# Kernel optimization log

Hardware: AMD Instinct MI355X
Metric: run time of the kernel (lower is better)

Reference implementation:

```python
import jax, jax.numpy as jnp
import numpy as np

B, N, D, H = 4, 1024, 1024, 16
DK = D // H
NEG_INF = jnp.finfo(jnp.float32).min


def setup_inputs() -> dict:
    key = jax.random.key(0)
    ks = jax.random.split(key, 6)
    x = jax.random.normal(ks[0], (B, N, D), dtype=jnp.float32)
    # padding mask: True where padded; vary lengths per batch element
    lengths = jnp.array([N, N - 128, N - 256, N - 512], dtype=jnp.int32)
    mask = jnp.arange(N)[None, :] >= lengths[:, None]  # [B, N] bool
    s = (1.0 / np.sqrt(D)).astype(np.float32)  # xavier-ish scale
    Wq = jax.random.normal(ks[1], (D, D), dtype=jnp.float32) * s
    Wk = jax.random.normal(ks[2], (D, D), dtype=jnp.float32) * s
    Wv = jax.random.normal(ks[3], (D, D), dtype=jnp.float32) * s
    Wo = jax.random.normal(ks[4], (D, D), dtype=jnp.float32) * s
    z = jnp.zeros((D,), dtype=jnp.float32)
    return {"x": x, "mask": mask, "Wq": Wq, "bq": z, "Wk": Wk, "bk": z,
            "Wv": Wv, "bv": z, "Wo": Wo, "bo": z}


def reference(x, mask, Wq, bq, Wk, bk, Wv, bv, Wo, bo):
    b, n, d = x.shape
    scale = jnp.asarray(DK, x.dtype) ** -0.5
    # QKV projections (weights stored [out, in] like torch Linear)
    def proj(W, bias):
        y = jnp.einsum('bnd,ed->bne', x, W) + bias
        return y.reshape(b, n, H, DK).transpose(0, 2, 1, 3)  # [B,H,N,Dk]
    q = proj(Wq, bq)
    k = proj(Wk, bk)
    v = proj(Wv, bv)
    energy = jnp.einsum('bhqd,bhkd->bhqk', q, k) * scale  # [B,H,N,N]
    energy = jnp.where(mask[:, None, None, :], NEG_INF, energy)
    weights = jax.nn.softmax(energy, axis=-1)
    attn = jnp.einsum('bhqk,bhkd->bhqd', weights, v)  # [B,H,N,Dk]
    attn = attn.transpose(0, 2, 1, 3).reshape(b, n, d)
    return jnp.einsum('bnd,ed->bne', attn, Wo) + bo
```

## Files before the change

kernel.cpp:

```cpp
#include <hip/hip_runtime.h>

#define DEV __device__ __forceinline__

typedef __attribute__((ext_vector_type(8))) short s16x8;
typedef __attribute__((ext_vector_type(4))) float f32x4;
typedef __attribute__((ext_vector_type(4))) unsigned short u16x4;
typedef __attribute__((ext_vector_type(2))) unsigned int u32x2;

static constexpr int Bb = 4, Nn = 1024, Dd = 1024, Hh = 16, DKk = 64;

DEV unsigned short f2bf(float f) {
    union { float f; unsigned int u; } x; x.f = f;
    unsigned int r = x.u + 0x7FFFu + ((x.u >> 16) & 1u);
    return (unsigned short)(r >> 16);
}

DEV float fexp2(float x) {
#if __has_builtin(__builtin_amdgcn_exp2f)
    return __builtin_amdgcn_exp2f(x);
#else
    return exp2f(x);
#endif
}

DEV void gld16(const void* g, void* l) {
    __builtin_amdgcn_global_load_lds(
        (const __attribute__((address_space(1))) void*)g,
        (__attribute__((address_space(3))) void*)l, 16, 0, 0);
}

DEV void wait_vm4_barrier() {
    __builtin_amdgcn_sched_barrier(0);
    asm volatile("s_waitcnt vmcnt(4)" ::: "memory");
    __builtin_amdgcn_sched_barrier(0);
    __builtin_amdgcn_s_barrier();
}

__global__ __launch_bounds__(256) void cast_k(const float* __restrict__ x,
                                              const float* __restrict__ Wq,
                                              const float* __restrict__ Wk,
                                              const float* __restrict__ Wv,
                                              const float* __restrict__ Wo,
                                              const unsigned int* __restrict__ mraw,
                                              unsigned short* __restrict__ xb,
                                              unsigned short* __restrict__ Wqb,
                                              unsigned short* __restrict__ Wkb,
                                              unsigned short* __restrict__ Wvb,
                                              unsigned short* __restrict__ Wob,
                                              int* __restrict__ lengths) {
    if (blockIdx.x == 4096) {
        __shared__ int is_u8;
        const int tid = threadIdx.x;
        if (tid == 0) is_u8 = 0;
        __syncthreads();
        int nz = 0;
        for (int i = tid; i < 1024; i += 256) nz |= (mraw[i] != 0u) ? 1 : 0;
        if (nz) is_u8 = 1;
        __syncthreads();
        const int wv = tid >> 6, lane = tid & 63;
        int cnt = 0;
        if (is_u8) {
            const unsigned char* b8 = (const unsigned char*)mraw;
            for (int n = lane; n < Nn; n += 64) cnt += (b8[wv * Nn + n] == 0) ? 1 : 0;
        } else {
            for (int n = lane; n < Nn; n += 64) cnt += (mraw[wv * Nn + n] == 0u) ? 1 : 0;
        }
#pragma unroll
        for (int off = 32; off; off >>= 1) cnt += __shfl_xor(cnt, off);
        if (lane == 0) lengths[wv] = cnt;
        return;
    }
    const size_t i = ((size_t)blockIdx.x * 256 + threadIdx.x) * 8;
    const float* src;
    unsigned short* dst;
    size_t off;
    const size_t XE = (size_t)4 * 1024 * 1024, WE = (size_t)1024 * 1024;
    if (i < XE) {
        src = x; dst = xb; off = i;
    } else {
        size_t j = i - XE;
        int w = (int)(j >> 20);
        off = j & (WE - 1);
        src = (w == 0) ? Wq : (w == 1) ? Wk : (w == 2) ? Wv : Wo;
        dst = (w == 0) ? Wqb : (w == 1) ? Wkb : (w == 2) ? Wvb : Wob;
    }
    f32x4 a = *(const f32x4*)(src + off);
    f32x4 b = *(const f32x4*)(src + off + 4);
    s16x8 t;
    t[0] = (short)f2bf(a[0]); t[1] = (short)f2bf(a[1]);
    t[2] = (short)f2bf(a[2]); t[3] = (short)f2bf(a[3]);
    t[4] = (short)f2bf(b[0]); t[5] = (short)f2bf(b[1]);
    t[6] = (short)f2bf(b[2]); t[7] = (short)f2bf(b[3]);
    *(s16x8*)(dst + off) = t;
}

DEV void gemm_kloop(const unsigned short* __restrict__ A,
                    const unsigned short* __restrict__ W,
                    char* lA, char* lB, int bm, int bn,
                    int tid, int kstep0, f32x4 (&acc)[4][4]) {
    const int wv = tid >> 6, lane = tid & 63, g = lane >> 4, lr = lane & 15;
    const int wr = wv >> 1, wc = wv & 1;

    const int rbase = wv * 8 + (lane >> 3);
    const int corig = (lane & 7) ^ (lane >> 3);
    const unsigned short* Asrc = A + (size_t)(bm + rbase) * Dd + corig * 8;
    const unsigned short* Bsrc = W + (size_t)(bn + rbase) * Dd + corig * 8;
    const int ldsb = wv * 1024;
    const int xk = (lr & 7);

    int kstep = kstep0;
    for (int it = 0; it < 16; ++it) {
        const int k0 = kstep * 64;
#pragma unroll
        for (int p = 0; p < 4; ++p) {
            gld16(Asrc + (size_t)(p * 32) * Dd + k0, lA + p * 4096 + ldsb);
            gld16(Bsrc + (size_t)(p * 32) * Dd + k0, lB + p * 4096 + ldsb);
        }
        __syncthreads();
#pragma unroll
        for (int s = 0; s < 2; ++s) {
            s16x8 af[4], bf[4];
#pragma unroll
            for (int m = 0; m < 4; ++m)
                af[m] = *(const s16x8*)(lA + (wr * 64 + m * 16 + lr) * 128 + (((s * 4 + g) ^ xk) << 4));
#pragma unroll
            for (int n = 0; n < 4; ++n)
                bf[n] = *(const s16x8*)(lB + (wc * 64 + n * 16 + lr) * 128 + (((s * 4 + g) ^ xk) << 4));
#pragma unroll
            for (int m = 0; m < 4; ++m)
#pragma unroll
                for (int n = 0; n < 4; ++n)
                    acc[m][n] = __builtin_amdgcn_mfma_f32_16x16x32_bf16(af[m], bf[n], acc[m][n], 0, 0, 0);
        }
        __syncthreads();
        kstep = (kstep + 1) & 15;
    }
}

__global__ __launch_bounds__(256, 4) void gemm_qkv_k(const unsigned short* __restrict__ xb,
                                                     const unsigned short* __restrict__ Wqb,
                                                     const unsigned short* __restrict__ Wkb,
                                                     const unsigned short* __restrict__ Wvb,
                                                     const float* __restrict__ bq,
                                                     const float* __restrict__ bk,
                                                     const float* __restrict__ bv,
                                                     unsigned short* __restrict__ Qo,
                                                     unsigned short* __restrict__ Ko,
                                                     unsigned short* __restrict__ Vo) {
    __shared__ __align__(16) char lA[128 * 64 * 2];
    __shared__ __align__(16) char lB[128 * 64 * 2];
    const int z = blockIdx.z;
    const unsigned short* W = (z == 0) ? Wqb : (z == 1) ? Wkb : Wvb;
    const float* bias = (z == 0) ? bq : (z == 1) ? bk : bv;

    const int tid = threadIdx.x;
    const int wv = tid >> 6, lane = tid & 63, g = lane >> 4, lr = lane & 15;
    const int wr = wv >> 1, wc = wv & 1;
    const int bm = blockIdx.x * 128, bn = blockIdx.y * 128;
    const int kstep0 = (blockIdx.x * 5 + blockIdx.y * 3 + z * 7) & 15;

    f32x4 acc[4][4];
#pragma unroll
    for (int m = 0; m < 4; ++m)
#pragma unroll
        for (int n = 0; n < 4; ++n) acc[m][n] = (f32x4){0.f, 0.f, 0.f, 0.f};

    gemm_kloop(xb, W, lA, lB, bm, bn, tid, kstep0, acc);

    const int row0 = bm + wr * 64 + g * 4;
    if (z == 0) {
        const float qs = 0.125f * 1.44269504f;
#pragma unroll
        for (int m = 0; m < 4; ++m)
#pragma unroll
            for (int n = 0; n < 4; ++n) {
                const int col = bn + wc * 64 + n * 16 + lr;
                const float bv_ = bias[col];
#pragma unroll
                for (int r = 0; r < 4; ++r)
                    Qo[(size_t)(row0 + m * 16 + r) * Dd + col] = f2bf((acc[m][n][r] + bv_) * qs);
            }
    } else if (z == 1) {
#pragma unroll
        for (int m = 0; m < 4; ++m)
#pragma unroll
            for (int n = 0; n < 4; ++n) {
                const int col = bn + wc * 64 + n * 16 + lr;
                const int h = col >> 6, dk = col & 63;
                const float bv_ = bias[col];
#pragma unroll
                for (int r = 0; r < 4; ++r) {
                    const int rowg = row0 + m * 16 + r;
                    const int b_ = rowg >> 10, tok = rowg & 1023;
                    size_t idx = ((size_t)(b_ * Hh + h) * Nn + tok) * DKk +
                                 (((dk >> 3) ^ (tok & 7)) << 3) + (dk & 7);
                    Ko[idx] = f2bf(acc[m][n][r] + bv_);
                }
            }
    } else {
#pragma unroll
        for (int m = 0; m < 4; ++m)
#pragma unroll
            for (int n = 0; n < 4; ++n) {
                const int col = bn + wc * 64 + n * 16 + lr;
                const int h = col >> 6, dk = col & 63;
                const float bv_ = bias[col];
                const int rowg = row0 + m * 16;
                const int b_ = rowg >> 10, tok = rowg & 1023;
                u16x4 t;
#pragma unroll
                for (int r = 0; r < 4; ++r) t[r] = f2bf(acc[m][n][r] + bv_);
                size_t idx = ((size_t)(b_ * Hh + h) * DKk + dk) * Nn + (tok & ~63) +
                             ((((tok >> 3) & 7) ^ (dk & 7)) << 3) + (tok & 7);
                *(u16x4*)(Vo + idx) = t;
            }
    }
}

__global__ __launch_bounds__(256, 4) void gemm_out_k(const unsigned short* __restrict__ Ab,
                                                     const unsigned short* __restrict__ Wob,
                                                     const float* __restrict__ bo,
                                                     float* __restrict__ out) {
    __shared__ __align__(16) char lA[128 * 64 * 2];
    __shared__ __align__(16) char lB[128 * 64 * 2];
    const int tid = threadIdx.x;
    const int wv = tid >> 6, lane = tid & 63, g = lane >> 4, lr = lane & 15;
    const int wr = wv >> 1, wc = wv & 1;
    const int bm = blockIdx.x * 128, bn = blockIdx.y * 128;
    const int kstep0 = (blockIdx.x * 5 + blockIdx.y * 3) & 15;

    f32x4 acc[4][4];
#pragma unroll
    for (int m = 0; m < 4; ++m)
#pragma unroll
        for (int n = 0; n < 4; ++n) acc[m][n] = (f32x4){0.f, 0.f, 0.f, 0.f};

    gemm_kloop(Ab, Wob, lA, lB, bm, bn, tid, kstep0, acc);

    const int row0 = bm + wr * 64 + g * 4;
#pragma unroll
    for (int m = 0; m < 4; ++m)
#pragma unroll
        for (int n = 0; n < 4; ++n) {
            const int col = bn + wc * 64 + n * 16 + lr;
            const float bv_ = bo[col];
#pragma unroll
            for (int r = 0; r < 4; ++r)
                out[(size_t)(row0 + m * 16 + r) * Dd + col] = acc[m][n][r] + bv_;
        }
}

__global__ __launch_bounds__(256) void attn_k(const unsigned short* __restrict__ Q,
                                              const unsigned short* __restrict__ Kg,
                                              const unsigned short* __restrict__ Vtg,
                                              const int* __restrict__ lengths,
                                              unsigned short* __restrict__ O) {
    const int tid = threadIdx.x;
    const int wv = tid >> 6, lane = tid & 63, g = lane >> 4, lr = lane & 15;
    const int bid = blockIdx.x;
    const int qt = bid & 15, h = (bid >> 4) & 15, b = bid >> 8;
    const int len = lengths[b];
    const int nt = (len + 63) >> 6;

    __shared__ __align__(16) char Ks[2 * 64 * 128];
    __shared__ __align__(16) char Vs[2 * 64 * 128];
    __shared__ __align__(16) char Ps[4][16 * 128];

    s16x8 qf[2];
    {
        const int qrow = b * Nn + qt * 64 + wv * 16 + lr;
        const unsigned short* qp = Q + (size_t)qrow * Dd + h * DKk + g * 8;
        qf[0] = *(const s16x8*)qp;
        qf[1] = *(const s16x8*)(qp + 32);
    }

    float m_run = 0.f, l_run = 0.f;
    f32x4 oacc[4];
#pragma unroll
    for (int dt = 0; dt < 4; ++dt) oacc[dt] = (f32x4){0.f, 0.f, 0.f, 0.f};

    const int s0 = wv * 64 + lane;
    const int r0 = s0 >> 3, c0 = s0 & 7;
    const int r1 = r0 + 32;
    const unsigned short* Kbase = Kg + (size_t)(b * Hh + h) * Nn * DKk;
    const unsigned short* Vbase = Vtg + (size_t)(b * Hh + h) * DKk * Nn;

    const int xk16 = (lr & 7) << 4;
    const int shsrc = (lane & 48) | (g * 4);

    gld16(Kbase + (size_t)r0 * DKk + c0 * 8, Ks + wv * 1024);
    gld16(Kbase + (size_t)r1 * DKk + c0 * 8, Ks + wv * 1024 + 4096);
    gld16(Vbase + (size_t)r0 * Nn + c0 * 8, Vs + wv * 1024);
    gld16(Vbase + (size_t)r1 * Nn + c0 * 8, Vs + wv * 1024 + 4096);

    int cur = 0;
    for (int kt = 0; kt < nt; ++kt) {
        const int kb = kt * 64;
        {
            const int kb2 = (kt + 1 < nt) ? kb + 64 : 0;
            const int nb = (cur ^ 1) * 8192;
            gld16(Kbase + (size_t)(kb2 + r0) * DKk + c0 * 8, Ks + nb + wv * 1024);
            gld16(Kbase + (size_t)(kb2 + r1) * DKk + c0 * 8, Ks + nb + wv * 1024 + 4096);
            gld16(Vbase + (size_t)r0 * Nn + kb2 + c0 * 8, Vs + nb + wv * 1024);
            gld16(Vbase + (size_t)r1 * Nn + kb2 + c0 * 8, Vs + nb + wv * 1024 + 4096);
        }
        wait_vm4_barrier();

        const char* ks_ = Ks + cur * 8192;
        const char* vs_ = Vs + cur * 8192;

        const float nm = -m_run;
        f32x4 sfr[4];
        __builtin_amdgcn_s_setprio(1);
#pragma unroll
        for (int ct = 0; ct < 4; ++ct) {
            f32x4 c = (f32x4){nm, nm, nm, nm};
#pragma unroll
            for (int s = 0; s < 2; ++s) {
                s16x8 kf = *(const s16x8*)(ks_ + (ct * 16 + lr) * 128 + ((((s * 4 + g) << 4)) ^ xk16));
                c = __builtin_amdgcn_mfma_f32_16x16x32_bf16(kf, qf[s], c, 0, 0, 0);
            }
            sfr[ct] = c;
        }
        __builtin_amdgcn_s_setprio(0);

        float mx = -INFINITY;
        if (kb + 64 <= len) {
#pragma unroll
            for (int ct = 0; ct < 4; ++ct)
#pragma unroll
                for (int r = 0; r < 4; ++r) mx = fmaxf(mx, sfr[ct][r]);
        } else {
#pragma unroll
            for (int ct = 0; ct < 4; ++ct) {
                const int kb4 = kb + ct * 16 + g * 4;
#pragma unroll
                for (int r = 0; r < 4; ++r) {
                    const float s_ = (kb4 + r < len) ? sfr[ct][r] : -INFINITY;
                    sfr[ct][r] = s_;
                    mx = fmaxf(mx, s_);
                }
            }
        }
        mx = fmaxf(mx, __shfl_xor(mx, 16));
        mx = fmaxf(mx, __shfl_xor(mx, 32));

        float ls = 0.f;
        if (__any(mx > 8.f)) {
            const float dm = fmaxf(mx, 0.f);
            const float alpha = fexp2(-dm);
            m_run += dm;
            l_run *= alpha;
            float ao[4];
#pragma unroll
            for (int r = 0; r < 4; ++r) ao[r] = __shfl(alpha, shsrc + r);
#pragma unroll
            for (int dt = 0; dt < 4; ++dt)
#pragma unroll
                for (int r = 0; r < 4; ++r) oacc[dt][r] *= ao[r];
#pragma unroll
            for (int ct = 0; ct < 4; ++ct)
#pragma unroll
                for (int r = 0; r < 4; ++r) {
                    const float p = fexp2(sfr[ct][r] - dm);
                    sfr[ct][r] = p;
                    ls += p;
                }
        } else {
#pragma unroll
            for (int ct = 0; ct < 4; ++ct)
#pragma unroll
                for (int r = 0; r < 4; ++r) {
                    const float p = fexp2(sfr[ct][r]);
                    sfr[ct][r] = p;
                    ls += p;
                }
        }
        ls += __shfl_xor(ls, 16);
        ls += __shfl_xor(ls, 32);
        l_run += ls;

#pragma unroll
        for (int ct = 0; ct < 4; ++ct) {
            unsigned int w0, w1;
            asm("v_cvt_pk_bf16_f32 %0, %1, %2" : "=v"(w0) : "v"(sfr[ct][0]), "v"(sfr[ct][1]));
            asm("v_cvt_pk_bf16_f32 %0, %1, %2" : "=v"(w1) : "v"(sfr[ct][2]), "v"(sfr[ct][3]));
            u32x2 wp; wp[0] = w0; wp[1] = w1;
            *(u32x2*)(Ps[wv] + lr * 128 + ((ct * 32 + g * 8) ^ xk16)) = wp;
        }

        __builtin_amdgcn_s_setprio(1);
#pragma unroll
        for (int s = 0; s < 2; ++s) {
            s16x8 pf = *(const s16x8*)(Ps[wv] + lr * 128 + ((((s * 4 + g) << 4)) ^ xk16));
#pragma unroll
            for (int dt = 0; dt < 4; ++dt) {
                s16x8 vf = *(const s16x8*)(vs_ + (dt * 16 + lr) * 128 + ((((s * 4 + g) << 4)) ^ xk16));
                oacc[dt] = __builtin_amdgcn_mfma_f32_16x16x32_bf16(pf, vf, oacc[dt], 0, 0, 0);
            }
        }
        __builtin_amdgcn_s_setprio(0);
        __builtin_amdgcn_s_barrier();
        cur ^= 1;
    }

    float lo[4];
#pragma unroll
    for (int r = 0; r < 4; ++r) lo[r] = __shfl(l_run, shsrc + r);
#pragma unroll
    for (int dt = 0; dt < 4; ++dt) {
        const int col = h * DKk + dt * 16 + lr;
#pragma unroll
        for (int r = 0; r < 4; ++r) {
            const int row = qt * 64 + wv * 16 + g * 4 + r;
            float v = oacc[dt][r] / lo[r];
            O[(size_t)(b * Nn + row) * Dd + col] = f2bf(v);
        }
    }
}

extern "C" void kernel_launch(void* const* d_in, const int* in_sizes, int n_in,
                              void* d_out, int out_size, void* d_ws, size_t ws_size,
                              hipStream_t stream) {
    const float* x  = (const float*)d_in[0];
    const unsigned int* mraw = (const unsigned int*)d_in[1];
    const float* Wq = (const float*)d_in[2];
    const float* bq = (const float*)d_in[3];
    const float* Wk = (const float*)d_in[4];
    const float* bk = (const float*)d_in[5];
    const float* Wv = (const float*)d_in[6];
    const float* bv = (const float*)d_in[7];
    const float* Wo = (const float*)d_in[8];
    const float* bo = (const float*)d_in[9];

    char* ws = (char*)d_ws;
    int* lengths        = (int*)ws;                      ws += 1 << 16;
    unsigned short* xb  = (unsigned short*)ws;           ws += (size_t)Bb * Nn * Dd * 2;
    unsigned short* Wqb = (unsigned short*)ws;           ws += (size_t)Dd * Dd * 2;
    unsigned short* Wkb = (unsigned short*)ws;           ws += (size_t)Dd * Dd * 2;
    unsigned short* Wvb = (unsigned short*)ws;           ws += (size_t)Dd * Dd * 2;
    unsigned short* Wob = (unsigned short*)ws;           ws += (size_t)Dd * Dd * 2;
    unsigned short* Qb  = (unsigned short*)ws;           ws += (size_t)Bb * Nn * Dd * 2;
    unsigned short* Kg  = (unsigned short*)ws;           ws += (size_t)Bb * Nn * Dd * 2;
    unsigned short* Vtg = (unsigned short*)ws;           ws += (size_t)Bb * Nn * Dd * 2;
    unsigned short* Ab  = (unsigned short*)ws;

    cast_k<<<4097, 256, 0, stream>>>(x, Wq, Wk, Wv, Wo, mraw,
                                     xb, Wqb, Wkb, Wvb, Wob, lengths);

    dim3 qkv_grid(Bb * Nn / 128, Dd / 128, 3);
    gemm_qkv_k<<<qkv_grid, 256, 0, stream>>>(xb, Wqb, Wkb, Wvb, bq, bk, bv, Qb, Kg, Vtg);

    attn_k<<<Bb * Hh * (Nn / 64), 256, 0, stream>>>(Qb, Kg, Vtg, lengths, Ab);

    dim3 out_grid(Bb * Nn / 128, Dd / 128);
    gemm_out_k<<<out_grid, 256, 0, stream>>>(Ab, Wob, bo, (float*)d_out);
}
```

Before: 93.73 us.

## Fuse QKV GEMM into one 256x192-tile double-buffered kernel with 512 threads

The three Q/K/V projections become a single GEMM over a concatenated weight (Wf, 3072 rows) using 256x192 tiles, 8 waves, and a double-buffered LDS pipeline. It waits with vmcnt(7) so the next tile's loads overlap the current MFMAs, and raises wave priority during the MFMA block. The aim is more reuse per tile and less global-load latency exposed at the per-iteration syncthreads. The shared gemm_kloop helper is inlined into the output GEMM. Wf is assumed to be contiguous Wq/Wk/Wv, which holds given the workspace layout, and the larger LDS footprint lowers occupancy.

```diff
diff --git a/kernel.cpp b/kernel.cpp
--- a/kernel.cpp
+++ b/kernel.cpp
@@ -32,6 +32,12 @@
 DEV void wait_vm4_barrier() {
     __builtin_amdgcn_sched_barrier(0);
     asm volatile("s_waitcnt vmcnt(4)" ::: "memory");
+    __builtin_amdgcn_sched_barrier(0);
+    __builtin_amdgcn_s_barrier();
+}
+DEV void wait_vm7_barrier() {
+    __builtin_amdgcn_sched_barrier(0);
+    asm volatile("s_waitcnt vmcnt(7)" ::: "memory");
     __builtin_amdgcn_sched_barrier(0);
     __builtin_amdgcn_s_barrier();
 }
@@ -94,126 +100,118 @@
     *(s16x8*)(dst + off) = t;
 }
 
-DEV void gemm_kloop(const unsigned short* __restrict__ A,
-                    const unsigned short* __restrict__ W,
-                    char* lA, char* lB, int bm, int bn,
-                    int tid, int kstep0, f32x4 (&acc)[4][4]) {
-    const int wv = tid >> 6, lane = tid & 63, g = lane >> 4, lr = lane & 15;
-    const int wr = wv >> 1, wc = wv & 1;
-
-    const int rbase = wv * 8 + (lane >> 3);
-    const int corig = (lane & 7) ^ (lane >> 3);
-    const unsigned short* Asrc = A + (size_t)(bm + rbase) * Dd + corig * 8;
-    const unsigned short* Bsrc = W + (size_t)(bn + rbase) * Dd + corig * 8;
-    const int ldsb = wv * 1024;
-    const int xk = (lr & 7);
-
-    int kstep = kstep0;
-    for (int it = 0; it < 16; ++it) {
-        const int k0 = kstep * 64;
-#pragma unroll
-        for (int p = 0; p < 4; ++p) {
-            gld16(Asrc + (size_t)(p * 32) * Dd + k0, lA + p * 4096 + ldsb);
-            gld16(Bsrc + (size_t)(p * 32) * Dd + k0, lB + p * 4096 + ldsb);
-        }
-        __syncthreads();
-#pragma unroll
-        for (int s = 0; s < 2; ++s) {
-            s16x8 af[4], bf[4];
-#pragma unroll
-            for (int m = 0; m < 4; ++m)
-                af[m] = *(const s16x8*)(lA + (wr * 64 + m * 16 + lr) * 128 + (((s * 4 + g) ^ xk) << 4));
-#pragma unroll
-            for (int n = 0; n < 4; ++n)
-                bf[n] = *(const s16x8*)(lB + (wc * 64 + n * 16 + lr) * 128 + (((s * 4 + g) ^ xk) << 4));
-#pragma unroll
-            for (int m = 0; m < 4; ++m)
-#pragma unroll
-                for (int n = 0; n < 4; ++n)
-                    acc[m][n] = __builtin_amdgcn_mfma_f32_16x16x32_bf16(af[m], bf[n], acc[m][n], 0, 0, 0);
-        }
-        __syncthreads();
-        kstep = (kstep + 1) & 15;
-    }
-}
-
-__global__ __launch_bounds__(256, 4) void gemm_qkv_k(const unsigned short* __restrict__ xb,
-                                                     const unsigned short* __restrict__ Wqb,
-                                                     const unsigned short* __restrict__ Wkb,
-                                                     const unsigned short* __restrict__ Wvb,
+__global__ __launch_bounds__(512, 2) void gemm_qkv_k(const unsigned short* __restrict__ xb,
+                                                     const unsigned short* __restrict__ Wf,
                                                      const float* __restrict__ bq,
                                                      const float* __restrict__ bk,
                                                      const float* __restrict__ bv,
                                                      unsigned short* __restrict__ Qo,
                                                      unsigned short* __restrict__ Ko,
                                                      unsigned short* __restrict__ Vo) {
-    __shared__ __align__(16) char lA[128 * 64 * 2];
-    __shared__ __align__(16) char lB[128 * 64 * 2];
-    const int z = blockIdx.z;
-    const unsigned short* W = (z == 0) ? Wqb : (z == 1) ? Wkb : Wvb;
-    const float* bias = (z == 0) ? bq : (z == 1) ? bk : bv;
-
+    __shared__ __align__(16) char lds[2 * 57344];
     const int tid = threadIdx.x;
     const int wv = tid >> 6, lane = tid & 63, g = lane >> 4, lr = lane & 15;
-    const int wr = wv >> 1, wc = wv & 1;
-    const int bm = blockIdx.x * 128, bn = blockIdx.y * 128;
-    const int kstep0 = (blockIdx.x * 5 + blockIdx.y * 3 + z * 7) & 15;
-
-    f32x4 acc[4][4];
-#pragma unroll
-    for (int m = 0; m < 4; ++m)
-#pragma unroll
-        for (int n = 0; n < 4; ++n) acc[m][n] = (f32x4){0.f, 0.f, 0.f, 0.f};
-
-    gemm_kloop(xb, W, lA, lB, bm, bn, tid, kstep0, acc);
-
-    const int row0 = bm + wr * 64 + g * 4;
-    if (z == 0) {
-        const float qs = 0.125f * 1.44269504f;
-#pragma unroll
-        for (int m = 0; m < 4; ++m)
-#pragma unroll
-            for (int n = 0; n < 4; ++n) {
-                const int col = bn + wc * 64 + n * 16 + lr;
-                const float bv_ = bias[col];
+    const int wr = wv >> 2, wc = wv & 3;
+    const int bm = blockIdx.x * 256, bn = blockIdx.y * 192;
+    const int kstep0 = (blockIdx.x * 5 + blockIdx.y * 3) & 15;
+
+    f32x4 acc[8][3];
+#pragma unroll
+    for (int m = 0; m < 8; ++m)
+#pragma unroll
+        for (int n = 0; n < 3; ++n) acc[m][n] = (f32x4){0.f, 0.f, 0.f, 0.f};
+
+    const int rbase = tid >> 3;
+    const int corig = (tid & 7) ^ ((tid >> 3) & 7);
+    const unsigned short* Asrc = xb + (size_t)(bm + rbase) * Dd + corig * 8;
+    const unsigned short* Bsrc = Wf + (size_t)(bn + rbase) * Dd + corig * 8;
+    const int dst = tid * 16;
+    const int xk = lr & 7;
+
+    int kstep = kstep0;
+    {
+        const int k0 = kstep * 64;
+#pragma unroll
+        for (int p = 0; p < 4; ++p)
+            gld16(Asrc + (size_t)(p * 64) * Dd + k0, lds + p * 8192 + dst);
+#pragma unroll
+        for (int p = 0; p < 3; ++p)
+            gld16(Bsrc + (size_t)(p * 64) * Dd + k0, lds + 32768 + p * 8192 + dst);
+    }
+    int cur = 0;
+    for (int it = 0; it < 16; ++it) {
+        const int knext = (kstep + 1) & 15;
+        const int k1 = knext * 64, nb = (cur ^ 1) * 57344;
+#pragma unroll
+        for (int p = 0; p < 4; ++p)
+            gld16(Asrc + (size_t)(p * 64) * Dd + k1, lds + nb + p * 8192 + dst);
+#pragma unroll
+        for (int p = 0; p < 3; ++p)
+            gld16(Bsrc + (size_t)(p * 64) * Dd + k1, lds + nb + 32768 + p * 8192 + dst);
+
+        wait_vm7_barrier();
+
+        const char* a_ = lds + cur * 57344;
+        const char* b_ = a_ + 32768;
+#pragma unroll
+        for (int s = 0; s < 2; ++s) {
+            s16x8 af[8], bf[3];
+#pragma unroll
+            for (int m = 0; m < 8; ++m)
+                af[m] = *(const s16x8*)(a_ + (wr * 128 + m * 16 + lr) * 128 + (((s * 4 + g) ^ xk) << 4));
+#pragma unroll
+            for (int n = 0; n < 3; ++n)
+                bf[n] = *(const s16x8*)(b_ + (wc * 48 + n * 16 + lr) * 128 + (((s * 4 + g) ^ xk) << 4));
+            __builtin_amdgcn_s_setprio(1);
+#pragma unroll
+            for (int m = 0; m < 8; ++m)
+#pragma unroll
+                for (int n = 0; n < 3; ++n)
+                    acc[m][n] = __builtin_amdgcn_mfma_f32_16x16x32_bf16(af[m], bf[n], acc[m][n], 0, 0, 0);
+            __builtin_amdgcn_s_setprio(0);
+        }
+        __builtin_amdgcn_s_barrier();
+        cur ^= 1;
+        kstep = knext;
+    }
+
+    const float qs = 0.125f * 1.44269504f;
+    const int row0 = bm + wr * 128 + g * 4;
+#pragma unroll
+    for (int m = 0; m < 8; ++m) {
+#pragma unroll
+        for (int n = 0; n < 3; ++n) {
+            const int col = bn + wc * 48 + n * 16 + lr;
+            const int z = col >> 10, cc = col & 1023;
+            if (z == 0) {
+                const float bv_ = bq[cc];
 #pragma unroll
                 for (int r = 0; r < 4; ++r)
-                    Qo[(size_t)(row0 + m * 16 + r) * Dd + col] = f2bf((acc[m][n][r] + bv_) * qs);
-            }
-    } else if (z == 1) {
-#pragma unroll
-        for (int m = 0; m < 4; ++m)
-#pragma unroll
-            for (int n = 0; n < 4; ++n) {
-                const int col = bn + wc * 64 + n * 16 + lr;
-                const int h = col >> 6, dk = col & 63;
-                const float bv_ = bias[col];
+                    Qo[(size_t)(row0 + m * 16 + r) * Dd + cc] = f2bf((acc[m][n][r] + bv_) * qs);
+            } else if (z == 1) {
+                const int h = cc >> 6, dk = cc & 63;
+                const float bv_ = bk[cc];
 #pragma unroll
                 for (int r = 0; r < 4; ++r) {
                     const int rowg = row0 + m * 16 + r;
-                    const int b_ = rowg >> 10, tok = rowg & 1023;
-                    size_t idx = ((size_t)(b_ * Hh + h) * Nn + tok) * DKk +
+                    const int b_i = rowg >> 10, tok = rowg & 1023;
+                    size_t idx = ((size_t)(b_i * Hh + h) * Nn + tok) * DKk +
                                  (((dk >> 3) ^ (tok & 7)) << 3) + (dk & 7);
                     Ko[idx] = f2bf(acc[m][n][r] + bv_);
                 }
-            }
-    } else {
-#pragma unroll
-        for (int m = 0; m < 4; ++m)
-#pragma unroll
-            for (int n = 0; n < 4; ++n) {
-                const int col = bn + wc * 64 + n * 16 + lr;
-                const int h = col >> 6, dk = col & 63;
-                const float bv_ = bias[col];
+            } else {
+                const int h = cc >> 6, dk = cc & 63;
+                const float bv_ = bv[cc];
                 const int rowg = row0 + m * 16;
-                const int b_ = rowg >> 10, tok = rowg & 1023;
+                const int b_i = rowg >> 10, tok = rowg & 1023;
                 u16x4 t;
 #pragma unroll
                 for (int r = 0; r < 4; ++r) t[r] = f2bf(acc[m][n][r] + bv_);
-                size_t idx = ((size_t)(b_ * Hh + h) * DKk + dk) * Nn + (tok & ~63) +
+                size_t idx = ((size_t)(b_i * Hh + h) * DKk + dk) * Nn + (tok & ~63) +
                              ((((tok >> 3) & 7) ^ (dk & 7)) << 3) + (tok & 7);
                 *(u16x4*)(Vo + idx) = t;
             }
+        }
     }
 }
 
@@ -235,7 +233,40 @@
 #pragma unroll
         for (int n = 0; n < 4; ++n) acc[m][n] = (f32x4){0.f, 0.f, 0.f, 0.f};
 
-    gemm_kloop(Ab, Wob, lA, lB, bm, bn, tid, kstep0, acc);
+    const int rbase = wv * 8 + (lane >> 3);
+    const int corig = (lane & 7) ^ (lane >> 3);
+    const unsigned short* Asrc = Ab + (size_t)(bm + rbase) * Dd + corig * 8;
+    const unsigned short* Bsrc = Wob + (size_t)(bn + rbase) * Dd + corig * 8;
+    const int ldsb = wv * 1024;
+    const int xk = (lr & 7);
+
+    int kstep = kstep0;
+    for (int it = 0; it < 16; ++it) {
+        const int k0 = kstep * 64;
+#pragma unroll
+        for (int p = 0; p < 4; ++p) {
+            gld16(Asrc + (size_t)(p * 32) * Dd + k0, lA + p * 4096 + ldsb);
+            gld16(Bsrc + (size_t)(p * 32) * Dd + k0, lB + p * 4096 + ldsb);
+        }
+        __syncthreads();
+#pragma unroll
+        for (int s = 0; s < 2; ++s) {
+            s16x8 af[4], bf[4];
+#pragma unroll
+            for (int m = 0; m < 4; ++m)
+                af[m] = *(const s16x8*)(lA + (wr * 64 + m * 16 + lr) * 128 + (((s * 4 + g) ^ xk) << 4));
+#pragma unroll
+            for (int n = 0; n < 4; ++n)
+                bf[n] = *(const s16x8*)(lB + (wc * 64 + n * 16 + lr) * 128 + (((s * 4 + g) ^ xk) << 4));
+#pragma unroll
+            for (int m = 0; m < 4; ++m)
+#pragma unroll
+                for (int n = 0; n < 4; ++n)
+                    acc[m][n] = __builtin_amdgcn_mfma_f32_16x16x32_bf16(af[m], bf[n], acc[m][n], 0, 0, 0);
+        }
+        __syncthreads();
+        kstep = (kstep + 1) & 15;
+    }
 
     const int row0 = bm + wr * 64 + g * 4;
 #pragma unroll
@@ -448,8 +479,8 @@
     cast_k<<<4097, 256, 0, stream>>>(x, Wq, Wk, Wv, Wo, mraw,
                                      xb, Wqb, Wkb, Wvb, Wob, lengths);
 
-    dim3 qkv_grid(Bb * Nn / 128, Dd / 128, 3);
-    gemm_qkv_k<<<qkv_grid, 256, 0, stream>>>(xb, Wqb, Wkb, Wvb, bq, bk, bv, Qb, Kg, Vtg);
+    dim3 qkv_grid(Bb * Nn / 256, 3072 / 192);
+    gemm_qkv_k<<<qkv_grid, 512, 0, stream>>>(xb, Wqb, bq, bk, bv, Qb, Kg, Vtg);
 
     attn_k<<<Bb * Hh * (Nn / 64), 256, 0, stream>>>(Qb, Kg, Vtg, lengths, Ab);
 
```

Result: no change. 94.85 us (+1.2%).
